# Performance work log

Hardware: AMD Instinct MI355X
Metric: run time of the kernel (lower is better)

Reference implementation:

```python
import jax, jax.numpy as jnp
import numpy as np

D_MODEL = 1024
NUM_HEADS = 16
DEPTH = D_MODEL // NUM_HEADS


def setup_inputs() -> dict:
    key = jax.random.key(0)
    ks = jax.random.split(key, 7)
    B, S = 2, 2048
    s = 0.02
    return {
        "q": jax.random.normal(ks[0], (B, S, D_MODEL), jnp.float32),
        "k": jax.random.normal(ks[1], (B, S, D_MODEL), jnp.float32),
        "v": jax.random.normal(ks[2], (B, S, D_MODEL), jnp.float32),
        "mask": jnp.zeros((B, 1, 1, S), jnp.float32),
        "wq": s * jax.random.normal(ks[3], (D_MODEL, D_MODEL), jnp.float32),
        "wk": s * jax.random.normal(ks[4], (D_MODEL, D_MODEL), jnp.float32),
        "wv": s * jax.random.normal(ks[5], (D_MODEL, D_MODEL), jnp.float32),
        "wo": s * jax.random.normal(ks[6], (D_MODEL, D_MODEL), jnp.float32),
    }


def _split_heads(x):
    # [B,S,D] -> [B,H,S,depth]
    B, S, _ = x.shape
    return x.reshape(B, S, NUM_HEADS, DEPTH).transpose(0, 2, 1, 3)


def reference(q, k, v, mask, wq, wk, wv, wo):
    B, S, _ = q.shape
    qh = _split_heads(q @ wq)
    kh = _split_heads(k @ wk)
    vh = _split_heads(v @ wv)
    # scaled dot-product attention: [B,H,S,S]
    scores = jnp.einsum('bhqd,bhkd->bhqk', qh, kh) / jnp.sqrt(jnp.float32(DEPTH))
    scores = scores + mask * -1e9
    attn = jax.nn.softmax(scores, axis=-1)
    out = jnp.einsum('bhqk,bhkd->bhqd', attn, vh)  # [B,H,S,depth]
    out = out.transpose(0, 2, 1, 3).reshape(B, S, D_MODEL)
    return out @ wo
```

## Files before the change

### kernel.cpp

```cpp
#include <hip/hip_runtime.h>

#define SEQ 2048
#define DM 1024
#define NH 16
#define HD 64
#define MTOT 4096

typedef float f32x4 __attribute__((ext_vector_type(4)));
typedef __bf16 bf16x8 __attribute__((ext_vector_type(8)));
typedef unsigned short u16x8 __attribute__((ext_vector_type(8)));
typedef unsigned short u16x4 __attribute__((ext_vector_type(4)));

__device__ __forceinline__ unsigned short f2bf(float f) {
  union { float f; unsigned u; } v; v.f = f;
  unsigned u = v.u + 0x7FFFu + ((v.u >> 16) & 1u);
  return (unsigned short)(u >> 16);
}

__device__ __forceinline__ f32x4 zero4() { f32x4 z = {0.f, 0.f, 0.f, 0.f}; return z; }

__device__ __forceinline__ f32x4 mfma16(bf16x8 a, bf16x8 b, f32x4 c) {
  return __builtin_amdgcn_mfma_f32_16x16x32_bf16(a, b, c, 0, 0, 0);
}

__global__ __launch_bounds__(256) void cvt_bf16(const float* __restrict__ in,
                                                unsigned short* __restrict__ out, int n8) {
  int i = blockIdx.x * 256 + threadIdx.x;
  if (i >= n8) return;
  const f32x4* p = (const f32x4*)(in + (size_t)i * 8);
  f32x4 a = p[0], b = p[1];
  u16x8 o;
  o[0] = f2bf(a[0]); o[1] = f2bf(a[1]); o[2] = f2bf(a[2]); o[3] = f2bf(a[3]);
  o[4] = f2bf(b[0]); o[5] = f2bf(b[1]); o[6] = f2bf(b[2]); o[7] = f2bf(b[3]);
  *(u16x8*)(out + (size_t)i * 8) = o;
}

__global__ __launch_bounds__(256) void wtrans(const float* __restrict__ wqp, const float* __restrict__ wkp,
                                              const float* __restrict__ wvp, const float* __restrict__ wop,
                                              unsigned short* __restrict__ wt) {
  const float* w = blockIdx.z == 0 ? wqp : blockIdx.z == 1 ? wkp : blockIdx.z == 2 ? wvp : wop;
  unsigned short* o = wt + (size_t)blockIdx.z * DM * DM;
  __shared__ float tile[64][65];
  const int t = threadIdx.x;
  const int k0 = blockIdx.y * 64, n0 = blockIdx.x * 64;
#pragma unroll
  for (int p = 0; p < 4; p++) {
    int r = p * 16 + (t >> 4), c = (t & 15) * 4;
    f32x4 v = *(const f32x4*)&w[(size_t)(k0 + r) * DM + n0 + c];
    tile[r][c] = v[0]; tile[r][c + 1] = v[1]; tile[r][c + 2] = v[2]; tile[r][c + 3] = v[3];
  }
  __syncthreads();
#pragma unroll
  for (int p = 0; p < 4; p++) {
    int r = p * 16 + (t >> 4), c = (t & 15) * 4;
    u16x4 ov;
    ov[0] = f2bf(tile[c][r]); ov[1] = f2bf(tile[c + 1][r]);
    ov[2] = f2bf(tile[c + 2][r]); ov[3] = f2bf(tile[c + 3][r]);
    *(u16x4*)&o[(size_t)(n0 + r) * DM + k0 + c] = ov;
  }
}

__device__ __forceinline__ void gemm_body(const unsigned short* __restrict__ A,
                                          const unsigned short* __restrict__ Bt,
                                          unsigned short* a_lds, unsigned short* b_lds,
                                          int m0, int n0, int K, f32x4 acc[4][4]) {
  const int t = threadIdx.x;
  const int lane = t & 63, wid = t >> 6;
  const int wr = wid >> 1, wc = wid & 1;
  const int l15 = lane & 15, lg = lane >> 4;
#pragma unroll
  for (int mi = 0; mi < 4; mi++)
#pragma unroll
    for (int ni = 0; ni < 4; ni++) acc[mi][ni] = zero4();

  const int ar = t >> 2, ac = (t & 3) * 8;
  const unsigned short* gA0 = A + (size_t)(m0 + ar) * K + ac;
  const unsigned short* gA1 = A + (size_t)(m0 + 64 + ar) * K + ac;
  const unsigned short* gB0 = Bt + (size_t)(n0 + ar) * K + ac;
  const unsigned short* gB1 = Bt + (size_t)(n0 + 64 + ar) * K + ac;
  unsigned short* sA0 = a_lds + ar * 32 + ac;
  unsigned short* sA1 = sA0 + 64 * 32;
  unsigned short* sB0 = b_lds + ar * 32 + ac;
  unsigned short* sB1 = sB0 + 64 * 32;
  const unsigned short* rA = a_lds + (wr * 64 + l15) * 32 + lg * 8;
  const unsigned short* rB = b_lds + (wc * 64 + l15) * 32 + lg * 8;

  for (int k0 = 0; k0 < K; k0 += 32) {
    u16x8 va0 = *(const u16x8*)(gA0 + k0);
    u16x8 va1 = *(const u16x8*)(gA1 + k0);
    u16x8 vb0 = *(const u16x8*)(gB0 + k0);
    u16x8 vb1 = *(const u16x8*)(gB1 + k0);
    __syncthreads();
    *(u16x8*)sA0 = va0; *(u16x8*)sA1 = va1;
    *(u16x8*)sB0 = vb0; *(u16x8*)sB1 = vb1;
    __syncthreads();
    bf16x8 am[4], bn[4];
#pragma unroll
    for (int mi = 0; mi < 4; mi++) am[mi] = *(const bf16x8*)(rA + mi * 512);
#pragma unroll
    for (int ni = 0; ni < 4; ni++) bn[ni] = *(const bf16x8*)(rB + ni * 512);
#pragma unroll
    for (int mi = 0; mi < 4; mi++)
#pragma unroll
      for (int ni = 0; ni < 4; ni++)
        acc[mi][ni] = mfma16(am[mi], bn[ni], acc[mi][ni]);
  }
}

__global__ __launch_bounds__(256, 2) void qkv_gemm(const unsigned short* __restrict__ xb,
                                                   const unsigned short* __restrict__ wt,
                                                   unsigned short* __restrict__ heads) {
  __shared__ __attribute__((aligned(16))) unsigned short a_lds[128 * 32];
  __shared__ __attribute__((aligned(16))) unsigned short b_lds[128 * 32];
  const int z = blockIdx.z;
  const unsigned short* A = xb + (size_t)z * MTOT * DM;
  const unsigned short* Bt = wt + (size_t)z * DM * DM;
  unsigned short* dst = heads + (size_t)z * MTOT * DM;
  const int m0 = blockIdx.y * 128, n0 = blockIdx.x * 128;
  f32x4 acc[4][4];
  gemm_body(A, Bt, a_lds, b_lds, m0, n0, DM, acc);
  const float scale = (z == 0) ? 0.125f : 1.0f;
  const int t = threadIdx.x, lane = t & 63, wid = t >> 6;
  const int wr = wid >> 1, wc = wid & 1, l15 = lane & 15, lg = lane >> 4;
#pragma unroll
  for (int mi = 0; mi < 4; mi++) {
    const int m = m0 + wr * 64 + mi * 16 + lg * 4;
#pragma unroll
    for (int ni = 0; ni < 4; ni++) {
      const int n = n0 + wc * 64 + ni * 16 + l15;
      const int h = n >> 6, d = n & 63;
#pragma unroll
      for (int r = 0; r < 4; r++) {
        const int mm = m + r;
        const int bb = mm >> 11, s = mm & 2047;
        dst[((size_t)(bb * NH + h) * SEQ + s) * HD + d] = f2bf(acc[mi][ni][r] * scale);
      }
    }
  }
}

__global__ __launch_bounds__(256, 2) void out_gemm(const unsigned short* __restrict__ ao,
                                                   const unsigned short* __restrict__ wot,
                                                   float* __restrict__ out) {
  __shared__ __attribute__((aligned(16))) unsigned short a_lds[128 * 32];
  __shared__ __attribute__((aligned(16))) unsigned short b_lds[128 * 32];
  const int m0 = blockIdx.y * 128, n0 = blockIdx.x * 128;
  f32x4 acc[4][4];
  gemm_body(ao, wot, a_lds, b_lds, m0, n0, DM, acc);
  const int t = threadIdx.x, lane = t & 63, wid = t >> 6;
  const int wr = wid >> 1, wc = wid & 1, l15 = lane & 15, lg = lane >> 4;
#pragma unroll
  for (int mi = 0; mi < 4; mi++) {
    const int m = m0 + wr * 64 + mi * 16 + lg * 4;
#pragma unroll
    for (int ni = 0; ni < 4; ni++) {
      const int n = n0 + wc * 64 + ni * 16 + l15;
#pragma unroll
      for (int r = 0; r < 4; r++)
        out[(size_t)(m + r) * DM + n] = acc[mi][ni][r];
    }
  }
}

__global__ __launch_bounds__(256, 2) void attn(const unsigned short* __restrict__ qh,
                                               const unsigned short* __restrict__ kh,
                                               const unsigned short* __restrict__ vh,
                                               const float* __restrict__ mask,
                                               unsigned short* __restrict__ ao) {
  __shared__ __attribute__((aligned(16))) unsigned short vt[64][40];
  __shared__ __attribute__((aligned(16))) unsigned short pl[4][16][40];
  const int t = threadIdx.x, lane = t & 63, wid = t >> 6;
  const int l15 = lane & 15, lg = lane >> 4;
  const int hh = blockIdx.y, bb = hh >> 4, h = hh & 15;
  const size_t hbase = (size_t)hh * SEQ * HD;
  const unsigned short* Qh = qh + hbase;
  const unsigned short* Kh = kh + hbase;
  const unsigned short* Vh = vh + hbase;
  const float* mrow = mask + bb * SEQ;
  const int qbase = blockIdx.x * 64 + wid * 16;

  bf16x8 aq0 = *(const bf16x8*)&Qh[(size_t)(qbase + l15) * HD + lg * 8];
  bf16x8 aq1 = *(const bf16x8*)&Qh[(size_t)(qbase + l15) * HD + 32 + lg * 8];

  f32x4 o[4];
#pragma unroll
  for (int dt = 0; dt < 4; dt++) o[dt] = zero4();
  float mr[4] = {-1e30f, -1e30f, -1e30f, -1e30f};
  float lr[4] = {0.f, 0.f, 0.f, 0.f};

  const int vrow = t >> 3, vc8 = (t & 7) * 8;

  for (int kt = 0; kt < SEQ / 32; kt++) {
    const int kb = kt * 32;
    u16x8 vv = *(const u16x8*)&Vh[(size_t)(kb + vrow) * HD + vc8];

    f32x4 s0 = zero4(), s1 = zero4();
    {
      bf16x8 k00 = *(const bf16x8*)&Kh[(size_t)(kb + l15) * HD + lg * 8];
      bf16x8 k01 = *(const bf16x8*)&Kh[(size_t)(kb + l15) * HD + 32 + lg * 8];
      s0 = mfma16(aq0, k00, s0);
      s0 = mfma16(aq1, k01, s0);
      bf16x8 k10 = *(const bf16x8*)&Kh[(size_t)(kb + 16 + l15) * HD + lg * 8];
      bf16x8 k11 = *(const bf16x8*)&Kh[(size_t)(kb + 16 + l15) * HD + 32 + lg * 8];
      s1 = mfma16(aq0, k10, s1);
      s1 = mfma16(aq1, k11, s1);
    }

    __syncthreads();
#pragma unroll
    for (int i = 0; i < 8; i++) vt[vc8 + i][vrow] = vv[i];

    const float mv0 = mrow[kb + l15] * -1e9f;
    const float mv1 = mrow[kb + 16 + l15] * -1e9f;

    float corr[4];
#pragma unroll
    for (int r = 0; r < 4; r++) {
      s0[r] += mv0; s1[r] += mv1;
      float v = fmaxf(s0[r], s1[r]);
      v = fmaxf(v, __shfl_xor(v, 1));
      v = fmaxf(v, __shfl_xor(v, 2));
      v = fmaxf(v, __shfl_xor(v, 4));
      v = fmaxf(v, __shfl_xor(v, 8));
      const float mn = fmaxf(mr[r], v);
      corr[r] = exp2f((mr[r] - mn) * 1.44269504f);
      mr[r] = mn;
      const float p0 = exp2f((s0[r] - mn) * 1.44269504f);
      const float p1 = exp2f((s1[r] - mn) * 1.44269504f);
      pl[wid][lg * 4 + r][l15] = f2bf(p0);
      pl[wid][lg * 4 + r][16 + l15] = f2bf(p1);
      float sum = p0 + p1;
      sum += __shfl_xor(sum, 1);
      sum += __shfl_xor(sum, 2);
      sum += __shfl_xor(sum, 4);
      sum += __shfl_xor(sum, 8);
      lr[r] = lr[r] * corr[r] + sum;
    }
#pragma unroll
    for (int dt = 0; dt < 4; dt++) {
      o[dt][0] *= corr[0]; o[dt][1] *= corr[1];
      o[dt][2] *= corr[2]; o[dt][3] *= corr[3];
    }
    __syncthreads();
    bf16x8 pa = *(const bf16x8*)&pl[wid][l15][lg * 8];
#pragma unroll
    for (int dt = 0; dt < 4; dt++) {
      bf16x8 bv = *(const bf16x8*)&vt[dt * 16 + l15][lg * 8];
      o[dt] = mfma16(pa, bv, o[dt]);
    }
  }

  float inv[4];
#pragma unroll
  for (int r = 0; r < 4; r++) inv[r] = 1.0f / lr[r];
#pragma unroll
  for (int dt = 0; dt < 4; dt++)
#pragma unroll
    for (int r = 0; r < 4; r++) {
      const int s = qbase + lg * 4 + r;
      ao[(size_t)(bb * SEQ + s) * DM + h * HD + dt * 16 + l15] = f2bf(o[dt][r] * inv[r]);
    }
}

extern "C" void kernel_launch(void* const* d_in, const int* in_sizes, int n_in,
                              void* d_out, int out_size, void* d_ws, size_t ws_size,
                              hipStream_t stream) {
  const float* q = (const float*)d_in[0];
  const float* k = (const float*)d_in[1];
  const float* v = (const float*)d_in[2];
  const float* mask = (const float*)d_in[3];
  const float* wq = (const float*)d_in[4];
  const float* wk = (const float*)d_in[5];
  const float* wv = (const float*)d_in[6];
  const float* wo = (const float*)d_in[7];
  float* out = (float*)d_out;

  const size_t SZX = (size_t)MTOT * DM;
  unsigned short* ws = (unsigned short*)d_ws;
  unsigned short* xb = ws;
  unsigned short* wt = xb + 3 * SZX;
  unsigned short* heads = wt + 4 * (size_t)DM * DM;
  unsigned short* ao = xb;
  const size_t need = (3 * SZX + 4 * (size_t)DM * DM + 3 * SZX) * sizeof(unsigned short);
  if (ws_size < need) return;

  cvt_bf16<<<dim3(2048), dim3(256), 0, stream>>>(q, xb, (int)(SZX / 8));
  cvt_bf16<<<dim3(2048), dim3(256), 0, stream>>>(k, xb + SZX, (int)(SZX / 8));
  cvt_bf16<<<dim3(2048), dim3(256), 0, stream>>>(v, xb + 2 * SZX, (int)(SZX / 8));
  wtrans<<<dim3(16, 16, 4), dim3(256), 0, stream>>>(wq, wk, wv, wo, wt);
  qkv_gemm<<<dim3(8, 32, 3), dim3(256), 0, stream>>>(xb, wt, heads);
  attn<<<dim3(32, 32), dim3(256), 0, stream>>>(heads, heads + SZX, heads + 2 * SZX, mask, ao);
  out_gemm<<<dim3(8, 32), dim3(256), 0, stream>>>(ao, wt + 3 * (size_t)DM * DM, out);
}
```

Baseline: 384.1 us.

## Stage K/V through swizzled LDS with double buffering and pre-transposed V

```diff
diff --git a/kernel.cpp b/kernel.cpp
--- a/kernel.cpp
+++ b/kernel.cpp
@@ -6,15 +6,26 @@
 #define HD 64
 #define MTOT 4096
 
+#ifndef __has_builtin
+#define __has_builtin(x) 0
+#endif
+#if __has_builtin(__builtin_amdgcn_global_load_lds)
+#define HAS_GLL 1
+#define GLL16(gsrc, ldst)                                    \
+  __builtin_amdgcn_global_load_lds(                          \
+      (const __attribute__((address_space(1))) void*)(gsrc), \
+      (__attribute__((address_space(3))) void*)(ldst), 16, 0, 0)
+#endif
+
 typedef float f32x4 __attribute__((ext_vector_type(4)));
 typedef __bf16 bf16x8 __attribute__((ext_vector_type(8)));
 typedef unsigned short u16x8 __attribute__((ext_vector_type(8)));
 typedef unsigned short u16x4 __attribute__((ext_vector_type(4)));
 
 __device__ __forceinline__ unsigned short f2bf(float f) {
-  union { float f; unsigned u; } v; v.f = f;
-  unsigned u = v.u + 0x7FFFu + ((v.u >> 16) & 1u);
-  return (unsigned short)(u >> 16);
+  union { __bf16 h; unsigned short u; } v;
+  v.h = (__bf16)f;
+  return v.u;
 }
 
 __device__ __forceinline__ f32x4 zero4() { f32x4 z = {0.f, 0.f, 0.f, 0.f}; return z; }
@@ -78,14 +89,22 @@
   const unsigned short* gA1 = A + (size_t)(m0 + 64 + ar) * K + ac;
   const unsigned short* gB0 = Bt + (size_t)(n0 + ar) * K + ac;
   const unsigned short* gB1 = Bt + (size_t)(n0 + 64 + ar) * K + ac;
-  unsigned short* sA0 = a_lds + ar * 32 + ac;
-  unsigned short* sA1 = sA0 + 64 * 32;
-  unsigned short* sB0 = b_lds + ar * 32 + ac;
-  unsigned short* sB1 = sB0 + 64 * 32;
+  unsigned short* sA0 = a_lds + t * 8;
+  unsigned short* sA1 = a_lds + 64 * 32 + t * 8;
+  unsigned short* sB0 = b_lds + t * 8;
+  unsigned short* sB1 = b_lds + 64 * 32 + t * 8;
   const unsigned short* rA = a_lds + (wr * 64 + l15) * 32 + lg * 8;
   const unsigned short* rB = b_lds + (wc * 64 + l15) * 32 + lg * 8;
 
   for (int k0 = 0; k0 < K; k0 += 32) {
+#ifdef HAS_GLL
+    __syncthreads();
+    GLL16(gA0 + k0, sA0);
+    GLL16(gA1 + k0, sA1);
+    GLL16(gB0 + k0, sB0);
+    GLL16(gB1 + k0, sB1);
+    __syncthreads();
+#else
     u16x8 va0 = *(const u16x8*)(gA0 + k0);
     u16x8 va1 = *(const u16x8*)(gA1 + k0);
     u16x8 vb0 = *(const u16x8*)(gB0 + k0);
@@ -94,6 +113,7 @@
     *(u16x8*)sA0 = va0; *(u16x8*)sA1 = va1;
     *(u16x8*)sB0 = vb0; *(u16x8*)sB1 = vb1;
     __syncthreads();
+#endif
     bf16x8 am[4], bn[4];
 #pragma unroll
     for (int mi = 0; mi < 4; mi++) am[mi] = *(const bf16x8*)(rA + mi * 512);
@@ -119,21 +139,38 @@
   const int m0 = blockIdx.y * 128, n0 = blockIdx.x * 128;
   f32x4 acc[4][4];
   gemm_body(A, Bt, a_lds, b_lds, m0, n0, DM, acc);
-  const float scale = (z == 0) ? 0.125f : 1.0f;
   const int t = threadIdx.x, lane = t & 63, wid = t >> 6;
   const int wr = wid >> 1, wc = wid & 1, l15 = lane & 15, lg = lane >> 4;
-#pragma unroll
-  for (int mi = 0; mi < 4; mi++) {
-    const int m = m0 + wr * 64 + mi * 16 + lg * 4;
-#pragma unroll
-    for (int ni = 0; ni < 4; ni++) {
-      const int n = n0 + wc * 64 + ni * 16 + l15;
-      const int h = n >> 6, d = n & 63;
-#pragma unroll
-      for (int r = 0; r < 4; r++) {
-        const int mm = m + r;
-        const int bb = mm >> 11, s = mm & 2047;
-        dst[((size_t)(bb * NH + h) * SEQ + s) * HD + d] = f2bf(acc[mi][ni][r] * scale);
+  if (z == 2) {
+#pragma unroll
+    for (int mi = 0; mi < 4; mi++) {
+      const int m = m0 + wr * 64 + mi * 16 + lg * 4;
+      const int bb = m >> 11, s = m & 2047;
+#pragma unroll
+      for (int ni = 0; ni < 4; ni++) {
+        const int n = n0 + wc * 64 + ni * 16 + l15;
+        const int h = n >> 6, d = n & 63;
+        u16x4 ov;
+#pragma unroll
+        for (int r = 0; r < 4; r++) ov[r] = f2bf(acc[mi][ni][r]);
+        *(u16x4*)&dst[((size_t)(bb * NH + h) * HD + d) * SEQ + s] = ov;
+      }
+    }
+  } else {
+    const float scale = (z == 0) ? 0.125f : 1.0f;
+#pragma unroll
+    for (int mi = 0; mi < 4; mi++) {
+      const int m = m0 + wr * 64 + mi * 16 + lg * 4;
+#pragma unroll
+      for (int ni = 0; ni < 4; ni++) {
+        const int n = n0 + wc * 64 + ni * 16 + l15;
+        const int h = n >> 6, d = n & 63;
+#pragma unroll
+        for (int r = 0; r < 4; r++) {
+          const int mm = m + r;
+          const int bb = mm >> 11, s = mm & 2047;
+          dst[((size_t)(bb * NH + h) * SEQ + s) * HD + d] = f2bf(acc[mi][ni][r] * scale);
+        }
       }
     }
   }
@@ -164,18 +201,19 @@
 
 __global__ __launch_bounds__(256, 2) void attn(const unsigned short* __restrict__ qh,
                                                const unsigned short* __restrict__ kh,
-                                               const unsigned short* __restrict__ vh,
+                                               const unsigned short* __restrict__ vht,
                                                const float* __restrict__ mask,
                                                unsigned short* __restrict__ ao) {
-  __shared__ __attribute__((aligned(16))) unsigned short vt[64][40];
-  __shared__ __attribute__((aligned(16))) unsigned short pl[4][16][40];
+  __shared__ __attribute__((aligned(16))) unsigned short klds[32 * 64];
+  __shared__ __attribute__((aligned(16))) unsigned short vlds[2][64 * 32];
+  __shared__ __attribute__((aligned(16))) __bf16 pl[4][16][40];
   const int t = threadIdx.x, lane = t & 63, wid = t >> 6;
   const int l15 = lane & 15, lg = lane >> 4;
   const int hh = blockIdx.y, bb = hh >> 4, h = hh & 15;
   const size_t hbase = (size_t)hh * SEQ * HD;
   const unsigned short* Qh = qh + hbase;
   const unsigned short* Kh = kh + hbase;
-  const unsigned short* Vh = vh + hbase;
+  const unsigned short* VhT = vht + hbase;
   const float* mrow = mask + bb * SEQ;
   const int qbase = blockIdx.x * 64 + wid * 16;
 
@@ -188,27 +226,53 @@
   float mr[4] = {-1e30f, -1e30f, -1e30f, -1e30f};
   float lr[4] = {0.f, 0.f, 0.f, 0.f};
 
-  const int vrow = t >> 3, vc8 = (t & 7) * 8;
+  const int krow = t >> 3, kc = t & 7;
+  const unsigned short* gK = &Kh[(size_t)krow * HD + kc * 8];
+  unsigned short* sK = &klds[krow * 64 + ((kc ^ (krow & 7)) * 8)];
+  const unsigned short* gV = &VhT[(size_t)(t >> 2) * SEQ + (t & 3) * 8];
+
+  const unsigned short* rK0a = &klds[l15 * 64 + ((lg ^ (l15 & 7)) * 8)];
+  const unsigned short* rK0b = &klds[l15 * 64 + (((4 + lg) ^ (l15 & 7)) * 8)];
+  const unsigned short* rK1a = &klds[(16 + l15) * 64 + ((lg ^ (l15 & 7)) * 8)];
+  const unsigned short* rK1b = &klds[(16 + l15) * 64 + (((4 + lg) ^ (l15 & 7)) * 8)];
+  const int pc0 = (((l15 >> 3) ^ lg) * 8) + (l15 & 7);
+  const int pc1 = ((((l15 >> 3) + 2) ^ lg) * 8) + (l15 & 7);
+  const int prc = (lg ^ ((l15 >> 2) & 3)) * 8;
+
+  u16x8 kreg = *(const u16x8*)gK;
+#ifdef HAS_GLL
+  GLL16(gV, &vlds[0][t * 8]);
+#else
+  { u16x8 vr = *(const u16x8*)gV; *(u16x8*)&vlds[0][t * 8] = vr; }
+#endif
 
   for (int kt = 0; kt < SEQ / 32; kt++) {
+    const int cur = kt & 1;
     const int kb = kt * 32;
-    u16x8 vv = *(const u16x8*)&Vh[(size_t)(kb + vrow) * HD + vc8];
+    __syncthreads();
+    *(u16x8*)sK = kreg;
+    __syncthreads();
+    if (kt + 1 < SEQ / 32) {
+      const int kb1 = kb + 32;
+      kreg = *(const u16x8*)(gK + (size_t)kb1 * HD);
+#ifdef HAS_GLL
+      GLL16(gV + kb1, &vlds[cur ^ 1][t * 8]);
+#else
+      { u16x8 vr = *(const u16x8*)(gV + kb1); *(u16x8*)&vlds[cur ^ 1][t * 8] = vr; }
+#endif
+    }
 
     f32x4 s0 = zero4(), s1 = zero4();
-    {
-      bf16x8 k00 = *(const bf16x8*)&Kh[(size_t)(kb + l15) * HD + lg * 8];
-      bf16x8 k01 = *(const bf16x8*)&Kh[(size_t)(kb + l15) * HD + 32 + lg * 8];
-      s0 = mfma16(aq0, k00, s0);
-      s0 = mfma16(aq1, k01, s0);
-      bf16x8 k10 = *(const bf16x8*)&Kh[(size_t)(kb + 16 + l15) * HD + lg * 8];
-      bf16x8 k11 = *(const bf16x8*)&Kh[(size_t)(kb + 16 + l15) * HD + 32 + lg * 8];
-      s1 = mfma16(aq0, k10, s1);
-      s1 = mfma16(aq1, k11, s1);
-    }
-
-    __syncthreads();
-#pragma unroll
-    for (int i = 0; i < 8; i++) vt[vc8 + i][vrow] = vv[i];
+    s0 = mfma16(aq0, *(const bf16x8*)rK0a, s0);
+    s0 = mfma16(aq1, *(const bf16x8*)rK0b, s0);
+    s1 = mfma16(aq0, *(const bf16x8*)rK1a, s1);
+    s1 = mfma16(aq1, *(const bf16x8*)rK1b, s1);
+
+    const unsigned short* vb = &vlds[cur][0];
+    bf16x8 bv0 = *(const bf16x8*)&vb[(0 * 16 + l15) * 32 + lg * 8];
+    bf16x8 bv1 = *(const bf16x8*)&vb[(1 * 16 + l15) * 32 + lg * 8];
+    bf16x8 bv2 = *(const bf16x8*)&vb[(2 * 16 + l15) * 32 + lg * 8];
+    bf16x8 bv3 = *(const bf16x8*)&vb[(3 * 16 + l15) * 32 + lg * 8];
 
     const float mv0 = mrow[kb + l15] * -1e9f;
     const float mv1 = mrow[kb + 16 + l15] * -1e9f;
@@ -227,8 +291,8 @@
       mr[r] = mn;
       const float p0 = exp2f((s0[r] - mn) * 1.44269504f);
       const float p1 = exp2f((s1[r] - mn) * 1.44269504f);
-      pl[wid][lg * 4 + r][l15] = f2bf(p0);
-      pl[wid][lg * 4 + r][16 + l15] = f2bf(p1);
+      pl[wid][lg * 4 + r][pc0] = (__bf16)p0;
+      pl[wid][lg * 4 + r][pc1] = (__bf16)p1;
       float sum = p0 + p1;
       sum += __shfl_xor(sum, 1);
       sum += __shfl_xor(sum, 2);
@@ -241,13 +305,11 @@
       o[dt][0] *= corr[0]; o[dt][1] *= corr[1];
       o[dt][2] *= corr[2]; o[dt][3] *= corr[3];
     }
-    __syncthreads();
-    bf16x8 pa = *(const bf16x8*)&pl[wid][l15][lg * 8];
-#pragma unroll
-    for (int dt = 0; dt < 4; dt++) {
-      bf16x8 bv = *(const bf16x8*)&vt[dt * 16 + l15][lg * 8];
-      o[dt] = mfma16(pa, bv, o[dt]);
-    }
+    bf16x8 pa = *(const bf16x8*)&pl[wid][l15][prc];
+    o[0] = mfma16(pa, bv0, o[0]);
+    o[1] = mfma16(pa, bv1, o[1]);
+    o[2] = mfma16(pa, bv2, o[2]);
+    o[3] = mfma16(pa, bv3, o[3]);
   }
 
   float inv[4];
```

Result: faster. 348.5 us (-9.3%).
